# Kernel tuning notes

Measured on AMD Instinct MI355X. Metric: run time of the kernel, lower is better.

## Reference

```python
import jax, jax.numpy as jnp
import numpy as np

N_NODES = 500000
N_EDGES = 1000000
H = 128


def setup_inputs() -> dict:
    key = jax.random.key(0)
    ks = jax.random.split(key, 8)
    s = 1.0 / np.sqrt(H)
    return {
        "z": jax.random.normal(ks[0], (N_NODES, H), dtype=jnp.float32),
        "w1": jax.random.normal(ks[1], (H, H), dtype=jnp.float32) * s,
        "b1": jax.random.normal(ks[2], (H,), dtype=jnp.float32) * s,
        "w2": jax.random.normal(ks[3], (H, H), dtype=jnp.float32) * s,
        "b2": jax.random.normal(ks[4], (H,), dtype=jnp.float32) * s,
        "wb": jax.random.normal(ks[5], (1, H, H), dtype=jnp.float32) * s,
        "bb": jax.random.normal(ks[6], (1,), dtype=jnp.float32) * s,
        "pot_arcs": jax.random.randint(ks[7], (N_EDGES, 2), 0, N_NODES, dtype=jnp.int64),
    }


def reference(z, w1, b1, w2, b2, wb, bb, pot_arcs):
    # Gather head/dep node embeddings per candidate arc: [E, H]
    x1 = z[pot_arcs[:, 0]]
    x2 = z[pot_arcs[:, 1]]
    # Per-node linear + relu (dropout is identity in eval mode)
    h1 = jax.nn.relu(x1 @ w1.T + b1)
    h2 = jax.nn.relu(x2 @ w2.T + b2)
    # Bilinear score: h1 @ W @ h2^T per edge, out_features=1
    score = jnp.einsum("eh,hk,ek->e", h1, wb[0], h2) + bb[0]
    return score
```

## Files before the change

kernel.cpp:

```cpp
#include <hip/hip_runtime.h>
#include <hip/hip_bf16.h>

#define HDIM 128

typedef short bf16x8 __attribute__((ext_vector_type(8)));
typedef unsigned short u16x8 __attribute__((ext_vector_type(8)));
typedef float f32x4 __attribute__((ext_vector_type(4)));

__device__ __forceinline__ short f2bf(float f) {
    __hip_bfloat16 h = __float2bfloat16(f);
    union { __hip_bfloat16 h; short s; } c; c.h = h; return c.s;
}
__device__ __forceinline__ float bf2f(unsigned short h) {
    union { unsigned u; float f; } c; c.u = ((unsigned)h) << 16; return c.f;
}
__device__ __forceinline__ bf16x8 pack8(float4 a, float4 b) {
    bf16x8 r;
    r[0] = f2bf(a.x); r[1] = f2bf(a.y); r[2] = f2bf(a.z); r[3] = f2bf(a.w);
    r[4] = f2bf(b.x); r[5] = f2bf(b.y); r[6] = f2bf(b.z); r[7] = f2bf(b.w);
    return r;
}

__device__ __forceinline__ void stage_T(const float* __restrict__ W, short* wfrag, int t) {
#pragma unroll
    for (int s = 0; s < 4; ++s) {
        int S = t + (s << 9);
        int f = S >> 6, sl = S & 63;
        int n  = ((f >> 2) << 4) + (sl & 15);
        int k0 = ((f & 3) << 5) + ((sl >> 4) << 3);
        const float* p = W + n * HDIM + k0;
        float4 a = *(const float4*)p;
        float4 b = *(const float4*)(p + 4);
        *(bf16x8*)&wfrag[S << 3] = pack8(a, b);
    }
}
__device__ __forceinline__ void stage_D(const float* __restrict__ W, short* wfrag, int t) {
#pragma unroll
    for (int s = 0; s < 4; ++s) {
        int S = t + (s << 9);
        int f = S >> 6, sl = S & 63;
        int n  = ((f >> 2) << 4) + (sl & 15);
        int k0 = ((f & 3) << 5) + ((sl >> 4) << 3);
        const float* p = W + (size_t)k0 * HDIM + n;
        bf16x8 r;
#pragma unroll
        for (int i = 0; i < 8; ++i) r[i] = f2bf(p[i * HDIM]);
        *(bf16x8*)&wfrag[S << 3] = r;
    }
}

__device__ __forceinline__ void run_gemm8(const short* wfrag, const bf16x8* a, f32x4* acc, int lane) {
#pragma unroll
    for (int kt = 0; kt < 4; ++kt) {
#pragma unroll
        for (int nt = 0; nt < 8; ++nt) {
            bf16x8 b = *(const bf16x8*)&wfrag[((((nt << 2) + kt) << 6) + lane) << 3];
            acc[nt] = __builtin_amdgcn_mfma_f32_16x16x32_bf16(a[kt], b, acc[nt], 0, 0, 0);
        }
    }
}

__global__ __launch_bounds__(512, 2)
void node_phase(const float* __restrict__ z,
                const float* __restrict__ w1, const float* __restrict__ b1,
                const float* __restrict__ w2, const float* __restrict__ b2,
                const float* __restrict__ wb,
                unsigned short* __restrict__ g1, unsigned short* __restrict__ h2o,
                int N)
{
    __shared__ short wf1[16384];
    __shared__ short wf2[16384];
    __shared__ short wfb[16384];
    __shared__ short rbuf[8 * 16 * HDIM];

    const int t = threadIdx.x;
    const int lane = t & 63, wid = t >> 6;
    const int l15 = lane & 15, kgrp = lane >> 4;

    stage_T(w1, wf1, t);
    stage_T(w2, wf2, t);
    stage_D(wb, wfb, t);

    float bias1[8], bias2[8];
#pragma unroll
    for (int nt = 0; nt < 8; ++nt) {
        bias1[nt] = b1[nt * 16 + l15];
        bias2[nt] = b2[nt * 16 + l15];
    }
    __syncthreads();

    const int ntiles = (N + 127) >> 7;
    const int wbase = wid * (16 * HDIM);

    float4 cur[8];
    int tile = blockIdx.x;
    if (tile < ntiles) {
        int m = tile * 128 + wid * 16 + l15;
        int mc = m < N ? m : N - 1;
        const float4* zr = (const float4*)(z + (size_t)mc * HDIM);
#pragma unroll
        for (int kt = 0; kt < 4; ++kt) {
            cur[2 * kt]     = zr[kt * 8 + kgrp * 2];
            cur[2 * kt + 1] = zr[kt * 8 + kgrp * 2 + 1];
        }
    }

    for (; tile < ntiles; tile += gridDim.x) {
        float4 nxt[8];
        int tnext = tile + gridDim.x;
        if (tnext < ntiles) {
            int m = tnext * 128 + wid * 16 + l15;
            int mc = m < N ? m : N - 1;
            const float4* zr = (const float4*)(z + (size_t)mc * HDIM);
#pragma unroll
            for (int kt = 0; kt < 4; ++kt) {
                nxt[2 * kt]     = zr[kt * 8 + kgrp * 2];
                nxt[2 * kt + 1] = zr[kt * 8 + kgrp * 2 + 1];
            }
        }

        bf16x8 za[4];
#pragma unroll
        for (int kt = 0; kt < 4; ++kt) za[kt] = pack8(cur[2 * kt], cur[2 * kt + 1]);

        const int mwave = tile * 128 + wid * 16;

        f32x4 acc[8];
#pragma unroll
        for (int nt = 0; nt < 8; ++nt) {
            float bv = bias1[nt];
            acc[nt] = (f32x4){bv, bv, bv, bv};
        }
        run_gemm8(wf1, za, acc, lane);
#pragma unroll
        for (int nt = 0; nt < 8; ++nt) {
#pragma unroll
            for (int r = 0; r < 4; ++r) {
                float v = acc[nt][r]; v = v > 0.f ? v : 0.f;
                int row = kgrp * 4 + r;
                int col = nt * 16 + l15;
                rbuf[wbase + row * HDIM + (col ^ ((row & 7) << 3))] = f2bf(v);
            }
        }

        f32x4 acc2[8];
#pragma unroll
        for (int nt = 0; nt < 8; ++nt) {
            float bv = bias2[nt];
            acc2[nt] = (f32x4){bv, bv, bv, bv};
        }
        run_gemm8(wf2, za, acc2, lane);

        bf16x8 a2[4];
#pragma unroll
        for (int kt = 0; kt < 4; ++kt) {
            int col = kt * 32 + kgrp * 8;
            a2[kt] = *(const bf16x8*)&rbuf[wbase + l15 * HDIM + (col ^ ((l15 & 7) << 3))];
        }
        asm volatile("s_waitcnt lgkmcnt(0)" ::: "memory");

#pragma unroll
        for (int nt = 0; nt < 8; ++nt) {
#pragma unroll
            for (int r = 0; r < 4; ++r) {
                float v = acc2[nt][r]; v = v > 0.f ? v : 0.f;
                int row = kgrp * 4 + r;
                int col = nt * 16 + l15;
                rbuf[wbase + row * HDIM + (col ^ ((row & 7) << 3))] = f2bf(v);
            }
        }
#pragma unroll
        for (int j = 0; j < 4; ++j) {
            int row = (lane >> 4) + 4 * j;
            int c0  = (lane & 15) * 8;
            u16x8 vv = *(const u16x8*)&rbuf[wbase + row * HDIM + (c0 ^ ((row & 7) << 3))];
            int m = mwave + row;
            if (m < N) *(u16x8*)&h2o[(size_t)m * HDIM + c0] = vv;
        }

        f32x4 accg[8];
#pragma unroll
        for (int nt = 0; nt < 8; ++nt) accg[nt] = (f32x4){0.f, 0.f, 0.f, 0.f};
        run_gemm8(wfb, a2, accg, lane);
        asm volatile("s_waitcnt lgkmcnt(0)" ::: "memory");
#pragma unroll
        for (int nt = 0; nt < 8; ++nt) {
#pragma unroll
            for (int r = 0; r < 4; ++r) {
                int row = kgrp * 4 + r;
                int col = nt * 16 + l15;
                rbuf[wbase + row * HDIM + (col ^ ((row & 7) << 3))] = f2bf(accg[nt][r]);
            }
        }
#pragma unroll
        for (int j = 0; j < 4; ++j) {
            int row = (lane >> 4) + 4 * j;
            int c0  = (lane & 15) * 8;
            u16x8 vv = *(const u16x8*)&rbuf[wbase + row * HDIM + (c0 ^ ((row & 7) << 3))];
            int m = mwave + row;
            if (m < N) *(u16x8*)&g1[(size_t)m * HDIM + c0] = vv;
        }

#pragma unroll
        for (int q = 0; q < 8; ++q) cur[q] = nxt[q];
    }
}

__global__ void detect_idx64(const int* __restrict__ arcs, int* __restrict__ flag)
{
    if (threadIdx.x == 0) {
        int is64 = 1;
        for (int j = 0; j < 64; ++j)
            if (arcs[2 * j + 1] != 0) { is64 = 0; break; }
        *flag = is64;
    }
}

__global__ __launch_bounds__(256, 8)
void edge_phase(const unsigned short* __restrict__ g1,
                const unsigned short* __restrict__ h2,
                const void* __restrict__ arcs,
                const int* __restrict__ flag,
                const float* __restrict__ bb,
                float* __restrict__ out, int E)
{
    const int t = threadIdx.x;
    const int sub = t & 15;
    const int e = blockIdx.x * 16 + (t >> 4);
    const int ec = e < E ? e : (E - 1);

    long long u, v;
    if (*flag) {
        const long long* a = (const long long*)arcs;
        u = a[2 * (size_t)ec]; v = a[2 * (size_t)ec + 1];
    } else {
        const int* a = (const int*)arcs;
        u = a[2 * (size_t)ec]; v = a[2 * (size_t)ec + 1];
    }

    u16x8 av = *(const u16x8*)(g1 + (size_t)u * HDIM + sub * 8);
    u16x8 bv = *(const u16x8*)(h2 + (size_t)v * HDIM + sub * 8);
    float s = 0.f;
#pragma unroll
    for (int i = 0; i < 8; ++i) s += bf2f(av[i]) * bf2f(bv[i]);

    s += __shfl_xor(s, 8, 16);
    s += __shfl_xor(s, 4, 16);
    s += __shfl_xor(s, 2, 16);
    s += __shfl_xor(s, 1, 16);

    if (sub == 0 && e < E) out[e] = s + bb[0];
}

extern "C" void kernel_launch(void* const* d_in, const int* in_sizes, int n_in,
                              void* d_out, int out_size, void* d_ws, size_t ws_size,
                              hipStream_t stream)
{
    const float* z  = (const float*)d_in[0];
    const float* w1 = (const float*)d_in[1];
    const float* b1 = (const float*)d_in[2];
    const float* w2 = (const float*)d_in[3];
    const float* b2 = (const float*)d_in[4];
    const float* wb = (const float*)d_in[5];
    const float* bb = (const float*)d_in[6];
    const void*  arcs = d_in[7];

    const int N = in_sizes[0] / HDIM;
    const int E = in_sizes[7] / 2;

    char* ws = (char*)d_ws;
    int* flag = (int*)ws;
    unsigned short* g1 = (unsigned short*)(ws + 256);
    unsigned short* h2 = g1 + (size_t)N * HDIM;

    detect_idx64<<<1, 64, 0, stream>>>((const int*)arcs, flag);

    node_phase<<<256, 512, 0, stream>>>(z, w1, b1, w2, b2, wb, g1, h2, N);

    int eblk = (E + 15) / 16;
    edge_phase<<<eblk, 256, 0, stream>>>(g1, h2, arcs, flag, bb, (float*)d_out, E);
}
```

Measured before the change: 194.6 us.

## Double node-phase block to 1024 threads with half-width per-wave LDS scratch

The node-phase kernel now runs 16 waves per block over 256-row tiles instead of 8 waves over 128 rows. Each wave's LDS scratch is halved to 16x64, so results go through it in two column halves. This keeps total shared memory the same while doubling the waves that share the staged weight fragments. The goal is more latency hiding for the z loads and MFMA work, at the cost of extra LDS round-trips and a possible register-pressure limit under launch_bounds(1024,4).

```diff
diff --git a/kernel.cpp b/kernel.cpp
--- a/kernel.cpp
+++ b/kernel.cpp
@@ -23,8 +23,8 @@
 
 __device__ __forceinline__ void stage_T(const float* __restrict__ W, short* wfrag, int t) {
 #pragma unroll
-    for (int s = 0; s < 4; ++s) {
-        int S = t + (s << 9);
+    for (int s = 0; s < 2; ++s) {
+        int S = t + (s << 10);
         int f = S >> 6, sl = S & 63;
         int n  = ((f >> 2) << 4) + (sl & 15);
         int k0 = ((f & 3) << 5) + ((sl >> 4) << 3);
@@ -36,8 +36,8 @@
 }
 __device__ __forceinline__ void stage_D(const float* __restrict__ W, short* wfrag, int t) {
 #pragma unroll
-    for (int s = 0; s < 4; ++s) {
-        int S = t + (s << 9);
+    for (int s = 0; s < 2; ++s) {
+        int S = t + (s << 10);
         int f = S >> 6, sl = S & 63;
         int n  = ((f >> 2) << 4) + (sl & 15);
         int k0 = ((f & 3) << 5) + ((sl >> 4) << 3);
@@ -60,7 +60,7 @@
     }
 }
 
-__global__ __launch_bounds__(512, 2)
+__global__ __launch_bounds__(1024, 4)
 void node_phase(const float* __restrict__ z,
                 const float* __restrict__ w1, const float* __restrict__ b1,
                 const float* __restrict__ w2, const float* __restrict__ b2,
@@ -71,11 +71,12 @@
     __shared__ short wf1[16384];
     __shared__ short wf2[16384];
     __shared__ short wfb[16384];
-    __shared__ short rbuf[8 * 16 * HDIM];
+    __shared__ short rbuf[16384];
 
     const int t = threadIdx.x;
     const int lane = t & 63, wid = t >> 6;
     const int l15 = lane & 15, kgrp = lane >> 4;
+    const int g8 = lane >> 3, s8 = lane & 7;
 
     stage_T(w1, wf1, t);
     stage_T(w2, wf2, t);
@@ -89,13 +90,13 @@
     }
     __syncthreads();
 
-    const int ntiles = (N + 127) >> 7;
-    const int wbase = wid * (16 * HDIM);
+    short* rb = &rbuf[wid << 10];
+    const int ntiles = (N + 255) >> 8;
 
     float4 cur[8];
     int tile = blockIdx.x;
     if (tile < ntiles) {
-        int m = tile * 128 + wid * 16 + l15;
+        int m = tile * 256 + wid * 16 + l15;
         int mc = m < N ? m : N - 1;
         const float4* zr = (const float4*)(z + (size_t)mc * HDIM);
 #pragma unroll
@@ -109,7 +110,7 @@
         float4 nxt[8];
         int tnext = tile + gridDim.x;
         if (tnext < ntiles) {
-            int m = tnext * 128 + wid * 16 + l15;
+            int m = tnext * 256 + wid * 16 + l15;
             int mc = m < N ? m : N - 1;
             const float4* zr = (const float4*)(z + (size_t)mc * HDIM);
 #pragma unroll
@@ -123,7 +124,7 @@
 #pragma unroll
         for (int kt = 0; kt < 4; ++kt) za[kt] = pack8(cur[2 * kt], cur[2 * kt + 1]);
 
-        const int mwave = tile * 128 + wid * 16;
+        const int mwave = tile * 256 + wid * 16;
 
         f32x4 acc[8];
 #pragma unroll
@@ -132,14 +133,25 @@
             acc[nt] = (f32x4){bv, bv, bv, bv};
         }
         run_gemm8(wf1, za, acc, lane);
-#pragma unroll
-        for (int nt = 0; nt < 8; ++nt) {
-#pragma unroll
-            for (int r = 0; r < 4; ++r) {
-                float v = acc[nt][r]; v = v > 0.f ? v : 0.f;
-                int row = kgrp * 4 + r;
-                int col = nt * 16 + l15;
-                rbuf[wbase + row * HDIM + (col ^ ((row & 7) << 3))] = f2bf(v);
+
+        bf16x8 a2[4];
+#pragma unroll
+        for (int p = 0; p < 2; ++p) {
+#pragma unroll
+            for (int nq = 0; nq < 4; ++nq) {
+                int nt = p * 4 + nq;
+#pragma unroll
+                for (int r = 0; r < 4; ++r) {
+                    float v = acc[nt][r]; v = v > 0.f ? v : 0.f;
+                    int row = kgrp * 4 + r;
+                    int col = nq * 16 + l15;
+                    rb[row * 64 + (col ^ ((row & 7) << 3))] = f2bf(v);
+                }
+            }
+#pragma unroll
+            for (int q = 0; q < 2; ++q) {
+                int col = q * 32 + kgrp * 8;
+                a2[p * 2 + q] = *(const bf16x8*)&rb[l15 * 64 + (col ^ ((l15 & 7) << 3))];
             }
         }
 
@@ -151,54 +163,54 @@
         }
         run_gemm8(wf2, za, acc2, lane);
 
-        bf16x8 a2[4];
-#pragma unroll
-        for (int kt = 0; kt < 4; ++kt) {
-            int col = kt * 32 + kgrp * 8;
-            a2[kt] = *(const bf16x8*)&rbuf[wbase + l15 * HDIM + (col ^ ((l15 & 7) << 3))];
-        }
         asm volatile("s_waitcnt lgkmcnt(0)" ::: "memory");
 
 #pragma unroll
-        for (int nt = 0; nt < 8; ++nt) {
-#pragma unroll
-            for (int r = 0; r < 4; ++r) {
-                float v = acc2[nt][r]; v = v > 0.f ? v : 0.f;
-                int row = kgrp * 4 + r;
-                int col = nt * 16 + l15;
-                rbuf[wbase + row * HDIM + (col ^ ((row & 7) << 3))] = f2bf(v);
-            }
-        }
-#pragma unroll
-        for (int j = 0; j < 4; ++j) {
-            int row = (lane >> 4) + 4 * j;
-            int c0  = (lane & 15) * 8;
-            u16x8 vv = *(const u16x8*)&rbuf[wbase + row * HDIM + (c0 ^ ((row & 7) << 3))];
-            int m = mwave + row;
-            if (m < N) *(u16x8*)&h2o[(size_t)m * HDIM + c0] = vv;
+        for (int p = 0; p < 2; ++p) {
+#pragma unroll
+            for (int nq = 0; nq < 4; ++nq) {
+                int nt = p * 4 + nq;
+#pragma unroll
+                for (int r = 0; r < 4; ++r) {
+                    float v = acc2[nt][r]; v = v > 0.f ? v : 0.f;
+                    int row = kgrp * 4 + r;
+                    int col = nq * 16 + l15;
+                    rb[row * 64 + (col ^ ((row & 7) << 3))] = f2bf(v);
+                }
+            }
+#pragma unroll
+            for (int q = 0; q < 2; ++q) {
+                int row = q * 8 + g8;
+                u16x8 vv = *(const u16x8*)&rb[row * 64 + ((s8 * 8) ^ ((row & 7) << 3))];
+                int m = mwave + row;
+                if (m < N) *(u16x8*)&h2o[(size_t)m * HDIM + p * 64 + s8 * 8] = vv;
+            }
         }
 
         f32x4 accg[8];
 #pragma unroll
         for (int nt = 0; nt < 8; ++nt) accg[nt] = (f32x4){0.f, 0.f, 0.f, 0.f};
         run_gemm8(wfb, a2, accg, lane);
-        asm volatile("s_waitcnt lgkmcnt(0)" ::: "memory");
-#pragma unroll
-        for (int nt = 0; nt < 8; ++nt) {
-#pragma unroll
-            for (int r = 0; r < 4; ++r) {
-                int row = kgrp * 4 + r;
-                int col = nt * 16 + l15;
-                rbuf[wbase + row * HDIM + (col ^ ((row & 7) << 3))] = f2bf(accg[nt][r]);
-            }
-        }
-#pragma unroll
-        for (int j = 0; j < 4; ++j) {
-            int row = (lane >> 4) + 4 * j;
-            int c0  = (lane & 15) * 8;
-            u16x8 vv = *(const u16x8*)&rbuf[wbase + row * HDIM + (c0 ^ ((row & 7) << 3))];
-            int m = mwave + row;
-            if (m < N) *(u16x8*)&g1[(size_t)m * HDIM + c0] = vv;
+
+#pragma unroll
+        for (int p = 0; p < 2; ++p) {
+#pragma unroll
+            for (int nq = 0; nq < 4; ++nq) {
+                int nt = p * 4 + nq;
+#pragma unroll
+                for (int r = 0; r < 4; ++r) {
+                    int row = kgrp * 4 + r;
+                    int col = nq * 16 + l15;
+                    rb[row * 64 + (col ^ ((row & 7) << 3))] = f2bf(accg[nt][r]);
+                }
+            }
+#pragma unroll
+            for (int q = 0; q < 2; ++q) {
+                int row = q * 8 + g8;
+                u16x8 vv = *(const u16x8*)&rb[row * 64 + ((s8 * 8) ^ ((row & 7) << 3))];
+                int m = mwave + row;
+                if (m < N) *(u16x8*)&g1[(size_t)m * HDIM + p * 64 + s8 * 8] = vv;
+            }
         }
 
 #pragma unroll
@@ -275,7 +287,7 @@
 
     detect_idx64<<<1, 64, 0, stream>>>((const int*)arcs, flag);
 
-    node_phase<<<256, 512, 0, stream>>>(z, w1, b1, w2, b2, wb, g1, h2, N);
+    node_phase<<<256, 1024, 0, stream>>>(z, w1, b1, w2, b2, wb, g1, h2, N);
 
     int eblk = (E + 15) / 16;
     edge_phase<<<eblk, 256, 0, stream>>>(g1, h2, arcs, flag, bb, (float*)d_out, E);
```

Measured after the change: 265.9 us. 36.6% more time.
